# Kernel optimization log

Hardware: AMD Instinct MI355X
Metric: run time of the kernel (lower is better)

Reference implementation:

```python
import jax, jax.numpy as jnp
import numpy as np

D_MODEL = 1024
NUM_HEADS = 16
D_K = D_MODEL // NUM_HEADS
THETA = 10000.0


def apply_rope(x, positions):
    # x: [b, h, s, d_k]; positions: [b, s] int32
    half = D_K // 2
    inv_freq = THETA ** (-jnp.arange(half, dtype=jnp.float32) * 2.0 / D_K)  # [half]
    angles = positions[:, None, :, None].astype(jnp.float32) * inv_freq  # [b,1,s,half]
    cos, sin = jnp.cos(angles), jnp.sin(angles)
    x1 = x[..., 0::2]  # even dims
    x2 = x[..., 1::2]  # odd dims
    out_even = x1 * cos - x2 * sin
    out_odd = x1 * sin + x2 * cos
    # re-interleave
    out = jnp.stack([out_even, out_odd], axis=-1)
    return out.reshape(x.shape)


def setup_inputs() -> dict:
    key = jax.random.key(0)
    ks = jax.random.split(key, 5)
    b, s = 2, 2048
    scale = 0.02
    return {
        "x": jax.random.normal(ks[0], (b, s, D_MODEL), dtype=jnp.float32),
        "Wq": jax.random.normal(ks[1], (D_MODEL, D_MODEL), dtype=jnp.float32) * scale,
        "Wk": jax.random.normal(ks[2], (D_MODEL, D_MODEL), dtype=jnp.float32) * scale,
        "Wv": jax.random.normal(ks[3], (D_MODEL, D_MODEL), dtype=jnp.float32) * scale,
        "Wo": jax.random.normal(ks[4], (D_MODEL, D_MODEL), dtype=jnp.float32) * scale,
    }


def reference(x, Wq, Wk, Wv, Wo):
    b, s, _ = x.shape
    # Linear(d, d) applied as x @ W^T (torch Linear convention, no bias)
    Q = x @ Wq.T
    K = x @ Wk.T
    V = x @ Wv.T
    # split heads: [b, s, h*d] -> [b, h, s, d]
    split = lambda t: t.reshape(b, s, NUM_HEADS, D_K).transpose(0, 2, 1, 3)
    Q, K, V = split(Q), split(K), split(V)
    positions = jnp.broadcast_to(jnp.arange(s, dtype=jnp.int32), (b, s))
    Q = apply_rope(Q, positions)
    K = apply_rope(K, positions)
    scores = jnp.einsum('bhqd,bhkd->bhqk', Q, K) / jnp.sqrt(jnp.float32(D_K))
    causal = jnp.tril(jnp.ones((s, s), dtype=bool))
    scores = jnp.where(causal[None, None], scores, -jnp.inf)
    attn = jax.nn.softmax(scores, axis=-1)
    out = jnp.einsum('bhqk,bhkd->bhqd', attn, V)
    out = out.transpose(0, 2, 1, 3).reshape(b, s, D_MODEL)
    return out @ Wo.T
```

## Files before the change

kernel.cpp:

```cpp
#include <hip/hip_runtime.h>

typedef __attribute__((ext_vector_type(8))) short bf16x8;
typedef __attribute__((ext_vector_type(4))) float f32x4;
typedef __attribute__((ext_vector_type(16))) float f32x16;

typedef const __attribute__((address_space(1))) unsigned int gu32;
typedef __attribute__((address_space(3))) unsigned int lu32;

__device__ __forceinline__ void async16(const void* g, void* l) {
  __builtin_amdgcn_global_load_lds((gu32*)g, (lu32*)l, 16, 0, 0);
}

__device__ __forceinline__ unsigned short f2bf(float f) {
  unsigned int u = __float_as_uint(f);
  u += 0x7fffu + ((u >> 16) & 1u);
  return (unsigned short)(u >> 16);
}
__device__ __forceinline__ float b2f(unsigned short s) {
  return __uint_as_float(((unsigned int)s) << 16);
}
__device__ __forceinline__ unsigned int cvtpk(float lo, float hi) {
  unsigned int w;
  asm("v_cvt_pk_bf16_f32 %0, %1, %2" : "=v"(w) : "v"(lo), "v"(hi));
  return w;
}
__device__ __forceinline__ void plswap(unsigned int& x, unsigned int& y) {
  asm("v_permlane32_swap_b32 %0, %1" : "+v"(x), "+v"(y));
}

__global__ __launch_bounds__(256) void cvt_k(const float* __restrict__ in,
                                             unsigned short* __restrict__ out,
                                             int n4) {
  int i = blockIdx.x * 256 + threadIdx.x;
  if (i >= n4) return;
  float4 v = ((const float4*)in)[i];
  ushort4 o;
  o.x = f2bf(v.x); o.y = f2bf(v.y); o.z = f2bf(v.z); o.w = f2bf(v.w);
  ((ushort4*)out)[i] = o;
}

template <int WRITE_F32>
__global__ __launch_bounds__(256) void gemm_bt(const unsigned short* __restrict__ A,
                                               const unsigned short* __restrict__ B,
                                               void* __restrict__ Cp, int N, int K) {
  __shared__ __align__(16) unsigned short Al[2][128 * 32];
  __shared__ __align__(16) unsigned short Bl[2][128 * 32];
  const int t = threadIdx.x;
  const int w = t >> 6, l = t & 63;
  const int wm = w >> 1, wn = w & 1;
  const int lr = l & 15, lg = l >> 4;
  const long bm = (long)blockIdx.x * 128, bn = (long)blockIdx.y * 128;
  const int srow = t >> 2;
  const int c8 = t & 3;
  const int KT = K >> 5;
  f32x4 acc[4][4] = {};

  auto STAGE = [&](int ts) {
    const int bi = ts & 1;
    const int k0 = ts * 32;
    #pragma unroll
    for (int r = 0; r < 2; ++r) {
      int row = r * 64 + srow;
      async16(&A[(bm + row) * (long)K + k0 + c8 * 8], &Al[bi][row * 32 + c8 * 8]);
      async16(&B[(bn + row) * (long)K + k0 + c8 * 8], &Bl[bi][row * 32 + c8 * 8]);
    }
  };

  STAGE(0);
  for (int kt = 0; kt < KT; ++kt) {
    const int cur = kt & 1;
    asm volatile("s_waitcnt vmcnt(0)" ::: "memory");
    __builtin_amdgcn_s_barrier();
    __builtin_amdgcn_sched_barrier(0);
    if (kt + 1 < KT) STAGE(kt + 1);
    bf16x8 af[4], bf[4];
    #pragma unroll
    for (int i = 0; i < 4; ++i) {
      af[i] = *(const bf16x8*)&Al[cur][(wm * 64 + i * 16 + lr) * 32 + lg * 8];
      bf[i] = *(const bf16x8*)&Bl[cur][(wn * 64 + i * 16 + lr) * 32 + lg * 8];
    }
    #pragma unroll
    for (int i = 0; i < 4; ++i)
      #pragma unroll
      for (int j = 0; j < 4; ++j)
        acc[i][j] = __builtin_amdgcn_mfma_f32_16x16x32_bf16(af[i], bf[j], acc[i][j], 0, 0, 0);
  }
  #pragma unroll
  for (int i = 0; i < 4; ++i)
    #pragma unroll
    for (int j = 0; j < 4; ++j)
      #pragma unroll
      for (int r = 0; r < 4; ++r) {
        long row = bm + wm * 64 + i * 16 + lg * 4 + r;
        long col = bn + wn * 64 + j * 16 + lr;
        float v = acc[i][j][r];
        if (WRITE_F32) ((float*)Cp)[row * N + col] = v;
        else ((unsigned short*)Cp)[row * N + col] = f2bf(v);
      }
}

__global__ __launch_bounds__(256) void rope_k(unsigned short* __restrict__ QKV) {
  __shared__ float csl[32], snl[32];
  const int row = blockIdx.x;
  const int s = row & 2047;
  const int t = threadIdx.x;
  if (t < 32) {
    float invf = exp2f((float)t * (-13.287712379549449f / 32.0f));
    float sn, cs;
    sincosf((float)s * invf, &sn, &cs);
    csl[t] = cs; snl[t] = sn;
  }
  __syncthreads();
  const int col0 = (t < 128) ? t * 8 : 1024 + (t - 128) * 8;
  const int i0 = (t & 7) * 4;
  unsigned short* p = &QKV[(size_t)row * 3072 + col0];
  bf16x8 v = *(const bf16x8*)p;
  bf16x8 o;
  #pragma unroll
  for (int j = 0; j < 4; ++j) {
    float x1 = b2f((unsigned short)v[2 * j]);
    float x2 = b2f((unsigned short)v[2 * j + 1]);
    float cs = csl[i0 + j], sn = snl[i0 + j];
    o[2 * j]     = (short)f2bf(x1 * cs - x2 * sn);
    o[2 * j + 1] = (short)f2bf(x1 * sn + x2 * cs);
  }
  *(bf16x8*)p = o;
}

__global__ __launch_bounds__(256) void vtr_k(const unsigned short* __restrict__ QKV,
                                             unsigned short* __restrict__ Vt) {
  __shared__ unsigned short tl[64][66];
  const int kt = blockIdx.x;
  const int bh = blockIdx.y;
  const int b = bh >> 4, h = bh & 15;
  const int t = threadIdx.x;
  const int row = t >> 3, c8 = t & 7;
  #pragma unroll
  for (int r = 0; r < 2; ++r) {
    int k = r * 32 + row;
    bf16x8 v = *(const bf16x8*)&QKV[((long)b * 2048 + kt * 64 + k) * 3072 + 2048 + h * 64 + c8 * 8];
    #pragma unroll
    for (int j = 0; j < 8; ++j) tl[c8 * 8 + j][k] = (unsigned short)v[j];
  }
  __syncthreads();
  #pragma unroll
  for (int r = 0; r < 2; ++r) {
    int d = r * 32 + row;
    ushort4 a, bq;
    a.x = tl[d][c8 * 8 + 0]; a.y = tl[d][c8 * 8 + 1];
    a.z = tl[d][c8 * 8 + 2]; a.w = tl[d][c8 * 8 + 3];
    bq.x = tl[d][c8 * 8 + 4]; bq.y = tl[d][c8 * 8 + 5];
    bq.z = tl[d][c8 * 8 + 6]; bq.w = tl[d][c8 * 8 + 7];
    long off = ((long)bh * 64 + d) * 2048 + kt * 64 + c8 * 8;
    *(ushort4*)&Vt[off] = a;
    *(ushort4*)&Vt[off + 4] = bq;
  }
}

__global__ __launch_bounds__(256) void attn_k(const unsigned short* __restrict__ QKV,
                                              const unsigned short* __restrict__ VtG,
                                              unsigned short* __restrict__ O) {
  __shared__ __align__(16) unsigned short Kl[3][64 * 64];
  __shared__ __align__(16) unsigned short Vl[3][64 * 64];
  const int t = threadIdx.x;
  const int w = t >> 6, l = t & 63;
  const int q31 = l & 31, hi = l >> 5;
  const int bh = blockIdx.x;
  const int qt = 15 - (int)blockIdx.y;
  const int b = bh >> 4, h = bh & 15;
  const int Qb = qt * 128;
  const long rowb = (long)b * 2048;
  const int L = 3072;
  const int NT = 2 * qt + 2;
  const float cexp = 0.125f * 1.4426950408889634f;

  const int qmy = Qb + 32 * w + q31;
  const long qgrow = rowb + qmy;
  const int ktmax = (Qb + 32 * w) >> 6;

  bf16x8 qf[4];
  #pragma unroll
  for (int dk = 0; dk < 4; ++dk)
    qf[dk] = *(const bf16x8*)&QKV[qgrow * L + h * 64 + dk * 16 + hi * 8];

  float m_ = -1e30f, ls = 0.0f;
  f32x16 oa[2];
  #pragma unroll
  for (int dt = 0; dt < 2; ++dt)
    #pragma unroll
    for (int r = 0; r < 16; ++r) oa[dt][r] = 0.0f;

  auto STAGE = [&](int ts) {
    const int bi = ts % 3;
    const long kb = rowb + (long)ts * 64;
    const long vrowb = (long)bh * 64;
    #pragma unroll
    for (int r = 0; r < 2; ++r) {
      int row = w * 16 + r * 8 + (l >> 3);
      int c8s = ((l & 7) ^ (row & 7)) * 8;
      async16(&QKV[(kb + row) * L + 1024 + h * 64 + c8s], &Kl[bi][row * 64 + (l & 7) * 8]);
      async16(&VtG[(vrowb + row) * 2048 + ts * 64 + c8s], &Vl[bi][row * 64 + (l & 7) * 8]);
    }
  };

  auto QK = [&](f32x16 (&st)[2], int bi) {
    #pragma unroll
    for (int kt2 = 0; kt2 < 2; ++kt2)
      #pragma unroll
      for (int r = 0; r < 16; ++r) st[kt2][r] = 0.0f;
    __builtin_amdgcn_s_setprio(1);
    #pragma unroll
    for (int dk = 0; dk < 4; ++dk)
      #pragma unroll
      for (int kt2 = 0; kt2 < 2; ++kt2) {
        int krow = kt2 * 32 + q31;
        bf16x8 kfr = *(const bf16x8*)&Kl[bi][krow * 64 + (((2 * dk + hi) ^ (krow & 7)) * 8)];
        st[kt2] = __builtin_amdgcn_mfma_f32_32x32x16_bf16(kfr, qf[dk], st[kt2], 0, 0, 0);
      }
    __builtin_amdgcn_s_setprio(0);
  };

  auto SMPV = [&](f32x16 (&st)[2], int kt) {
    if (kt == ktmax) {
      #pragma unroll
      for (int kt2 = 0; kt2 < 2; ++kt2)
        #pragma unroll
        for (int r = 0; r < 16; ++r) {
          int kg = kt * 64 + kt2 * 32 + (r & 3) + 8 * (r >> 2) + 4 * hi;
          if (kg > qmy) st[kt2][r] = -1e30f;
        }
    }
    float m0[8];
    #pragma unroll
    for (int i = 0; i < 8; ++i)
      m0[i] = fmaxf(fmaxf(st[0][i], st[0][i + 8]), fmaxf(st[1][i], st[1][i + 8]));
    float mt = fmaxf(fmaxf(fmaxf(m0[0], m0[1]), fmaxf(m0[2], m0[3])),
                     fmaxf(fmaxf(m0[4], m0[5]), fmaxf(m0[6], m0[7])));
    if (__any((mt - m_) * cexp > 8.0f)) {
      float mg = fmaxf(mt, __shfl_xor(mt, 32, 64));
      float mn = fmaxf(m_, mg);
      float al = __builtin_amdgcn_exp2f((m_ - mn) * cexp);
      m_ = mn;
      ls *= al;
      #pragma unroll
      for (int dt = 0; dt < 2; ++dt)
        #pragma unroll
        for (int r = 0; r < 16; ++r) oa[dt][r] *= al;
    }
    const float mc = m_ * cexp;
    #pragma unroll
    for (int kt2 = 0; kt2 < 2; ++kt2)
      #pragma unroll
      for (int r = 0; r < 16; ++r)
        st[kt2][r] = __builtin_amdgcn_exp2f(fmaf(st[kt2][r], cexp, -mc));
    float s0[8];
    #pragma unroll
    for (int i = 0; i < 8; ++i)
      s0[i] = (st[0][i] + st[0][i + 8]) + (st[1][i] + st[1][i + 8]);
    ls += ((s0[0] + s0[1]) + (s0[2] + s0[3])) + ((s0[4] + s0[5]) + (s0[6] + s0[7]));
    bf16x8 pfr[4];
    #pragma unroll
    for (int ks = 0; ks < 4; ++ks) {
      int tt = ks >> 1, gX = 2 * (ks & 1), gY = gX + 1;
      unsigned int x1 = cvtpk(st[tt][4 * gX + 0], st[tt][4 * gX + 1]);
      unsigned int y1 = cvtpk(st[tt][4 * gY + 0], st[tt][4 * gY + 1]);
      plswap(x1, y1);
      unsigned int x2 = cvtpk(st[tt][4 * gX + 2], st[tt][4 * gX + 3]);
      unsigned int y2 = cvtpk(st[tt][4 * gY + 2], st[tt][4 * gY + 3]);
      plswap(x2, y2);
      union { unsigned int u[4]; bf16x8 b; } cc;
      cc.u[0] = x1; cc.u[1] = x2; cc.u[2] = y1; cc.u[3] = y2;
      pfr[ks] = cc.b;
    }
    const int vb = kt % 3;
    __builtin_amdgcn_s_setprio(1);
    #pragma unroll
    for (int dt = 0; dt < 2; ++dt)
      #pragma unroll
      for (int ks = 0; ks < 4; ++ks) {
        int vrow = dt * 32 + q31;
        bf16x8 vf = *(const bf16x8*)&Vl[vb][vrow * 64 + (((2 * ks + hi) ^ (vrow & 7)) * 8)];
        oa[dt] = __builtin_amdgcn_mfma_f32_32x32x16_bf16(vf, pfr[ks], oa[dt], 0, 0, 0);
      }
    __builtin_amdgcn_s_setprio(0);
  };

  f32x16 stA[2], stB[2];

  STAGE(0);
  STAGE(1);
  asm volatile("s_waitcnt vmcnt(4)" ::: "memory");
  __builtin_amdgcn_s_barrier();
  __builtin_amdgcn_sched_barrier(0);
  QK(stA, 0);

  auto STEP = [&](f32x16 (&cur)[2], f32x16 (&nxt)[2], int kt) {
    asm volatile("s_waitcnt vmcnt(0)" ::: "memory");
    __builtin_amdgcn_s_barrier();
    __builtin_amdgcn_sched_barrier(0);
    if (kt + 1 < NT && kt + 1 <= ktmax) QK(nxt, (kt + 1) % 3);
    if (kt + 2 < NT) STAGE(kt + 2);
    if (kt <= ktmax) SMPV(cur, kt);
  };

  int kt = 0;
  while (kt < NT) {
    STEP(stA, stB, kt); ++kt;
    if (kt < NT) { STEP(stB, stA, kt); ++kt; }
  }

  float lt = ls + __shfl_xor(ls, 32, 64);
  float inv = 1.0f / lt;
  #pragma unroll
  for (int dt = 0; dt < 2; ++dt)
    #pragma unroll
    for (int g = 0; g < 4; ++g) {
      ushort4 o4;
      o4.x = f2bf(oa[dt][4 * g + 0] * inv);
      o4.y = f2bf(oa[dt][4 * g + 1] * inv);
      o4.z = f2bf(oa[dt][4 * g + 2] * inv);
      o4.w = f2bf(oa[dt][4 * g + 3] * inv);
      *(ushort4*)&O[qgrow * 1024 + h * 64 + dt * 32 + 8 * g + 4 * hi] = o4;
    }
}

extern "C" void kernel_launch(void* const* d_in, const int* in_sizes, int n_in,
                              void* d_out, int out_size, void* d_ws, size_t ws_size,
                              hipStream_t stream) {
  const float* x  = (const float*)d_in[0];
  const float* Wq = (const float*)d_in[1];
  const float* Wk = (const float*)d_in[2];
  const float* Wv = (const float*)d_in[3];
  const float* Wo = (const float*)d_in[4];
  char* ws = (char*)d_ws;
  unsigned short* xb   = (unsigned short*)(ws);
  unsigned short* Wb   = (unsigned short*)(ws + (8u << 20));
  unsigned short* Wob  = (unsigned short*)(ws + (14u << 20));
  unsigned short* QKVb = (unsigned short*)(ws + (16u << 20));
  unsigned short* Ob   = (unsigned short*)(ws + (40u << 20));
  unsigned short* Vtg  = xb;

  cvt_k<<<4096, 256, 0, stream>>>(x, xb, 4096 * 1024 / 4);
  cvt_k<<<1024, 256, 0, stream>>>(Wq, Wb, 1024 * 1024 / 4);
  cvt_k<<<1024, 256, 0, stream>>>(Wk, Wb + 1024 * 1024, 1024 * 1024 / 4);
  cvt_k<<<1024, 256, 0, stream>>>(Wv, Wb + 2 * 1024 * 1024, 1024 * 1024 / 4);
  cvt_k<<<1024, 256, 0, stream>>>(Wo, Wob, 1024 * 1024 / 4);

  gemm_bt<0><<<dim3(32, 24), 256, 0, stream>>>(xb, Wb, QKVb, 3072, 1024);
  rope_k<<<4096, 256, 0, stream>>>(QKVb);
  vtr_k<<<dim3(32, 32), 256, 0, stream>>>(QKVb, Vtg);
  attn_k<<<dim3(32, 16), 256, 0, stream>>>(QKVb, Vtg, Ob);
  gemm_bt<1><<<dim3(32, 8), 256, 0, stream>>>(Ob, Wob, d_out, 1024, 1024);
}
```

Measured before the change: 131.0 us.

## Compute softmax row sums via MFMA with ones, use max3, reorder query tiles

Replaces the VALU reduction of the softmax denominator with an extra MFMA that multiplies a ones matrix by the P fragments, so the row sum accumulates on the matrix cores. Max reductions use v_max3_f32, and the query-tile order per block.y alternates between heavy and light causal tiles. The extra MFMA adds matrix-core work and sixteen accumulator registers, and the sum now comes from bf16-rounded probabilities, which changes numerics slightly.

```diff
diff --git a/kernel.cpp b/kernel.cpp
--- a/kernel.cpp
+++ b/kernel.cpp
@@ -26,6 +26,11 @@
 }
 __device__ __forceinline__ void plswap(unsigned int& x, unsigned int& y) {
   asm("v_permlane32_swap_b32 %0, %1" : "+v"(x), "+v"(y));
+}
+__device__ __forceinline__ float max3f(float a, float b, float c) {
+  float d;
+  asm("v_max3_f32 %0, %1, %2, %3" : "=v"(d) : "v"(a), "v"(b), "v"(c));
+  return d;
 }
 
 __global__ __launch_bounds__(256) void cvt_k(const float* __restrict__ in,
@@ -166,7 +171,8 @@
   const int w = t >> 6, l = t & 63;
   const int q31 = l & 31, hi = l >> 5;
   const int bh = blockIdx.x;
-  const int qt = 15 - (int)blockIdx.y;
+  const int y = (int)blockIdx.y;
+  const int qt = (y < 8) ? (15 - y) : (y - 8);
   const int b = bh >> 4, h = bh & 15;
   const int Qb = qt * 128;
   const long rowb = (long)b * 2048;
@@ -183,12 +189,14 @@
   for (int dk = 0; dk < 4; ++dk)
     qf[dk] = *(const bf16x8*)&QKV[qgrow * L + h * 64 + dk * 16 + hi * 8];
 
-  float m_ = -1e30f, ls = 0.0f;
-  f32x16 oa[2];
-  #pragma unroll
-  for (int dt = 0; dt < 2; ++dt)
-    #pragma unroll
-    for (int r = 0; r < 16; ++r) oa[dt][r] = 0.0f;
+  bf16x8 onesf;
+  #pragma unroll
+  for (int j = 0; j < 8; ++j) onesf[j] = (short)0x3F80;
+
+  float m_ = -1e30f;
+  f32x16 oa[2], la;
+  #pragma unroll
+  for (int r = 0; r < 16; ++r) { oa[0][r] = 0.0f; oa[1][r] = 0.0f; la[r] = 0.0f; }
 
   auto STAGE = [&](int ts) {
     const int bi = ts % 3;
@@ -233,15 +241,15 @@
     float m0[8];
     #pragma unroll
     for (int i = 0; i < 8; ++i)
-      m0[i] = fmaxf(fmaxf(st[0][i], st[0][i + 8]), fmaxf(st[1][i], st[1][i + 8]));
-    float mt = fmaxf(fmaxf(fmaxf(m0[0], m0[1]), fmaxf(m0[2], m0[3])),
-                     fmaxf(fmaxf(m0[4], m0[5]), fmaxf(m0[6], m0[7])));
+      m0[i] = max3f(st[0][i], st[0][i + 8], fmaxf(st[1][i], st[1][i + 8]));
+    float mt = max3f(max3f(m0[0], m0[1], m0[2]), max3f(m0[3], m0[4], m0[5]),
+                     fmaxf(m0[6], m0[7]));
     if (__any((mt - m_) * cexp > 8.0f)) {
       float mg = fmaxf(mt, __shfl_xor(mt, 32, 64));
       float mn = fmaxf(m_, mg);
       float al = __builtin_amdgcn_exp2f((m_ - mn) * cexp);
       m_ = mn;
-      ls *= al;
+      la[0] *= al;
       #pragma unroll
       for (int dt = 0; dt < 2; ++dt)
         #pragma unroll
@@ -253,11 +261,6 @@
       #pragma unroll
       for (int r = 0; r < 16; ++r)
         st[kt2][r] = __builtin_amdgcn_exp2f(fmaf(st[kt2][r], cexp, -mc));
-    float s0[8];
-    #pragma unroll
-    for (int i = 0; i < 8; ++i)
-      s0[i] = (st[0][i] + st[0][i + 8]) + (st[1][i] + st[1][i + 8]);
-    ls += ((s0[0] + s0[1]) + (s0[2] + s0[3])) + ((s0[4] + s0[5]) + (s0[6] + s0[7]));
     bf16x8 pfr[4];
     #pragma unroll
     for (int ks = 0; ks < 4; ++ks) {
@@ -275,13 +278,15 @@
     const int vb = kt % 3;
     __builtin_amdgcn_s_setprio(1);
     #pragma unroll
-    for (int dt = 0; dt < 2; ++dt)
-      #pragma unroll
-      for (int ks = 0; ks < 4; ++ks) {
+    for (int ks = 0; ks < 4; ++ks) {
+      la = __builtin_amdgcn_mfma_f32_32x32x16_bf16(onesf, pfr[ks], la, 0, 0, 0);
+      #pragma unroll
+      for (int dt = 0; dt < 2; ++dt) {
         int vrow = dt * 32 + q31;
         bf16x8 vf = *(const bf16x8*)&Vl[vb][vrow * 64 + (((2 * ks + hi) ^ (vrow & 7)) * 8)];
         oa[dt] = __builtin_amdgcn_mfma_f32_32x32x16_bf16(vf, pfr[ks], oa[dt], 0, 0, 0);
       }
+    }
     __builtin_amdgcn_s_setprio(0);
   };
 
@@ -309,8 +314,7 @@
     if (kt < NT) { STEP(stB, stA, kt); ++kt; }
   }
 
-  float lt = ls + __shfl_xor(ls, 32, 64);
-  float inv = 1.0f / lt;
+  float inv = 1.0f / la[0];
   #pragma unroll
   for (int dt = 0; dt < 2; ++dt)
     #pragma unroll
```

Result: no change. 130.4 us (-0.5%).
